# Kernel optimization log

Measured on AMD Instinct MI355X. Metric: run time of the kernel, lower is better.

Reference implementation:

```python
import math
import jax, jax.numpy as jnp
import numpy as np

B, S, D = 8, 1024, 768
N_HEAD, D_HEAD = 12, 64


def setup_inputs() -> dict:
    key = jax.random.key(0)
    k1, k2, k3, k4, k5 = jax.random.split(key, 5)
    return {
        "x": jax.random.normal(k1, (B, S, D), dtype=jnp.float32),
        "W_qkv": jax.random.normal(k2, (D, 3 * D), dtype=jnp.float32) * 0.02,
        "b_qkv": jax.random.normal(k3, (3 * D,), dtype=jnp.float32) * 0.02,
        "W_proj": jax.random.normal(k4, (D, D), dtype=jnp.float32) * 0.02,
        "b_proj": jax.random.normal(k5, (D,), dtype=jnp.float32) * 0.02,
    }


def reference(x, W_qkv, b_qkv, W_proj, b_proj):
    b, s, d = x.shape
    qkv = x @ W_qkv + b_qkv                      # [B,S,3D]
    q, k, v = jnp.split(qkv, 3, axis=-1)
    # [B,S,D] -> [B,H,S,Dh]
    q = q.reshape(b, s, N_HEAD, D_HEAD).transpose(0, 2, 1, 3)
    k = k.reshape(b, s, N_HEAD, D_HEAD).transpose(0, 2, 1, 3)
    v = v.reshape(b, s, N_HEAD, D_HEAD).transpose(0, 2, 1, 3)
    scores = jnp.einsum("bhqd,bhkd->bhqk", q, k) / math.sqrt(D_HEAD)
    causal = jnp.tril(jnp.ones((s, s), dtype=bool))  # [S,S]
    scores = jnp.where(causal[None, None], scores, -jnp.inf)
    probs = jax.nn.softmax(scores, axis=-1)
    out = jnp.einsum("bhqk,bhkd->bhqd", probs, v)    # [B,H,S,Dh]
    out = out.transpose(0, 2, 1, 3).reshape(b, s, d)
    out = out @ W_proj + b_proj
    return out, (k, v)
```

## Files before the change

kernel.cpp:

```cpp
#include <hip/hip_runtime.h>

typedef unsigned short u16;
typedef unsigned int   u32;
typedef short bf16x8 __attribute__((ext_vector_type(8)));
typedef float f32x4  __attribute__((ext_vector_type(4)));
typedef float f32x16 __attribute__((ext_vector_type(16)));
typedef u16   u16x4  __attribute__((ext_vector_type(4)));
typedef u16   u16x8  __attribute__((ext_vector_type(8)));
typedef u32   u32x2  __attribute__((ext_vector_type(2)));
typedef u32   u32x4  __attribute__((ext_vector_type(4)));

#define DEV __device__ __forceinline__
#define MFMA32(A,B,C) __builtin_amdgcn_mfma_f32_32x32x16_bf16(A,B,C,0,0,0)

DEV u16 f2bf(float f) {
  u32 u = __builtin_bit_cast(u32, f);
  u32 r = (u + 0x7FFFu + ((u >> 16) & 1u)) >> 16;
  return (u16)r;
}
DEV u32 pack2(float lo, float hi) {
  return (u32)f2bf(lo) | ((u32)f2bf(hi) << 16);
}
DEV void gll16(const u16* g, u16* l) {
  __builtin_amdgcn_global_load_lds((const __attribute__((address_space(1))) u32*)g,
                                   (__attribute__((address_space(3))) u32*)l,
                                   16, 0, 0);
}

__global__ __launch_bounds__(256)
void cvt_bf16(const float* __restrict__ in, u16* __restrict__ out, int n8) {
  int i = blockIdx.x * 256 + threadIdx.x;
  if (i >= n8) return;
  float4 a = ((const float4*)in)[2*i];
  float4 b = ((const float4*)in)[2*i+1];
  u16x8 o;
  o[0]=f2bf(a.x); o[1]=f2bf(a.y); o[2]=f2bf(a.z); o[3]=f2bf(a.w);
  o[4]=f2bf(b.x); o[5]=f2bf(b.y); o[6]=f2bf(b.z); o[7]=f2bf(b.w);
  *(u16x8*)(out + (size_t)i*8) = o;
}

__global__ __launch_bounds__(256)
void transpose_w(const float* __restrict__ in, u16* __restrict__ out, int R, int C) {
  __shared__ float t64[64][65];
  const int r0 = blockIdx.x*64, c0 = blockIdx.y*64;
  const int tr = threadIdx.x >> 4, tc = (threadIdx.x & 15) * 4;
  #pragma unroll
  for (int i = 0; i < 4; ++i) {
    int r = i*16 + tr;
    float4 v = *(const float4*)(in + (size_t)(r0 + r)*C + c0 + tc);
    t64[r][tc+0]=v.x; t64[r][tc+1]=v.y; t64[r][tc+2]=v.z; t64[r][tc+3]=v.w;
  }
  __syncthreads();
  #pragma unroll
  for (int i = 0; i < 4; ++i) {
    int r = i*16 + tr;
    u16x4 ov;
    ov[0]=f2bf(t64[tc+0][r]); ov[1]=f2bf(t64[tc+1][r]);
    ov[2]=f2bf(t64[tc+2][r]); ov[3]=f2bf(t64[tc+3][r]);
    *(u16x4*)(out + (size_t)(c0 + r)*R + r0 + tc) = ov;
  }
}

template<int MODE>
__global__ __launch_bounds__(256)
void gemm_k(const u16* __restrict__ A, const u16* __restrict__ Bt,
            const float* __restrict__ bias,
            float* __restrict__ o0, float* __restrict__ o1,
            u16* __restrict__ qo, u16* __restrict__ ko)
{
  constexpr int K = 768;
  __shared__ u16 As[128*32];
  __shared__ u16 Bs[128*32];
  const int tid = threadIdx.x;
  const int w  = tid >> 6, ln = tid & 63;
  const int wr = w >> 1,  wc = w & 1;
  const int g  = ln >> 4, c  = ln & 15;
  const int tm = blockIdx.x * 128, tn = blockIdx.y * 128;

  const f32x4 fzero = {0.f, 0.f, 0.f, 0.f};
  f32x4 acc[4][4];
  #pragma unroll
  for (int i = 0; i < 4; ++i)
    #pragma unroll
    for (int j = 0; j < 4; ++j) acc[i][j] = fzero;

  const int srow = w*32 + (ln >> 2);
  const int seg  = (ln & 3) * 8;
  const u16* ga = A  + (size_t)(tm + srow)*K + seg;
  const u16* gb = Bt + (size_t)(tn + srow)*K + seg;
  u16* lA = As + __builtin_amdgcn_readfirstlane(w * 1024);
  u16* lB = Bs + __builtin_amdgcn_readfirstlane(w * 1024);

  for (int k0 = 0; k0 < K; k0 += 32) {
    gll16(ga + k0,        lA);
    gll16(ga + k0 + 16*K, lA + 512);
    gll16(gb + k0,        lB);
    gll16(gb + k0 + 16*K, lB + 512);
    __syncthreads();
    bf16x8 af[4], bfv[4];
    #pragma unroll
    for (int mi = 0; mi < 4; ++mi)
      af[mi] = *(const bf16x8*)&As[(wr*64 + mi*16 + c)*32 + g*8];
    #pragma unroll
    for (int ni = 0; ni < 4; ++ni)
      bfv[ni] = *(const bf16x8*)&Bs[(wc*64 + ni*16 + c)*32 + g*8];
    #pragma unroll
    for (int mi = 0; mi < 4; ++mi)
      #pragma unroll
      for (int ni = 0; ni < 4; ++ni)
        acc[mi][ni] = __builtin_amdgcn_mfma_f32_16x16x32_bf16(af[mi], bfv[ni], acc[mi][ni], 0, 0, 0);
    __syncthreads();
  }

  const int tnw = tn + wc*64;
  float bias_v[4];
  #pragma unroll
  for (int ni = 0; ni < 4; ++ni) bias_v[ni] = bias[tnw + ni*16 + c];

  if (MODE == 1) {
    #pragma unroll
    for (int mi = 0; mi < 4; ++mi)
      #pragma unroll
      for (int r = 0; r < 4; ++r) {
        int mrow = tm + wr*64 + mi*16 + 4*g + r;
        float* op = o0 + (size_t)mrow*768 + tnw + c;
        #pragma unroll
        for (int ni = 0; ni < 4; ++ni)
          op[ni*16] = acc[mi][ni][r] + bias_v[ni];
      }
  } else {
    const float QSCALE = 0.18033688f;
    const int part = tnw / 768;
    const int hh   = (tnw - part*768) >> 6;
    #pragma unroll
    for (int mi = 0; mi < 4; ++mi)
      #pragma unroll
      for (int r = 0; r < 4; ++r) {
        int mrow = tm + wr*64 + mi*16 + 4*g + r;
        int bI = mrow >> 10, s = mrow & 1023;
        size_t base = (((size_t)(bI*12 + hh) << 10) + (size_t)s) * 64 + c;
        #pragma unroll
        for (int ni = 0; ni < 4; ++ni) {
          float v = acc[mi][ni][r] + bias_v[ni];
          size_t idx = base + ni*16;
          if (part == 0)      { qo[idx] = f2bf(v * QSCALE); }
          else if (part == 1) { o0[idx] = v; ko[idx] = f2bf(v); }
          else                { o1[idx] = v; }
        }
      }
  }
}

__global__ __launch_bounds__(256)
void transpose_v(const float* __restrict__ vin, u16* __restrict__ vt) {
  __shared__ float t64[64][65];
  const int bh = blockIdx.x, s0 = blockIdx.y * 64;
  const int tr = threadIdx.x >> 4, tc = (threadIdx.x & 15) * 4;
  const float* src = vin + ((size_t)bh*1024 + s0) * 64;
  #pragma unroll
  for (int i = 0; i < 4; ++i) {
    int r = i*16 + tr;
    float4 v = *(const float4*)(src + (size_t)r*64 + tc);
    t64[r][tc+0]=v.x; t64[r][tc+1]=v.y; t64[r][tc+2]=v.z; t64[r][tc+3]=v.w;
  }
  __syncthreads();
  u16* dst = vt + (size_t)bh*64*1024 + s0;
  #pragma unroll
  for (int i = 0; i < 4; ++i) {
    int d = i*16 + tr;
    u16x4 ov;
    ov[0]=f2bf(t64[tc+0][d]); ov[1]=f2bf(t64[tc+1][d]);
    ov[2]=f2bf(t64[tc+2][d]); ov[3]=f2bf(t64[tc+3][d]);
    *(u16x4*)(dst + (size_t)d*1024 + tc) = ov;
  }
}


#define LOADT(KF, VF, TI) do {                                              \
  const int k32_ = (TI) << 5;                                               \
  const u16* kp_ = kb + hbase + (size_t)(k32_ + cl) * 64 + (hf << 3);       \
  KF[0] = *(const bf16x8*)(kp_);       KF[1] = *(const bf16x8*)(kp_ + 16);  \
  KF[2] = *(const bf16x8*)(kp_ + 32);  KF[3] = *(const bf16x8*)(kp_ + 48);  \
  const u16* vp_ = vt + hbase + (size_t)cl * 1024 + k32_ + (hf << 3);       \
  VF[0] = *(const bf16x8*)(vp_);           VF[1] = *(const bf16x8*)(vp_ + 16); \
  VF[2] = *(const bf16x8*)(vp_ + 32768);   VF[3] = *(const bf16x8*)(vp_ + 32768 + 16); \
} while (0)

#define TILE(KF, VF, DIAG) do {                                             \
  f32x16 st_ = 0.f;                                                         \
  st_ = MFMA32(KF[0], qf[0], st_); st_ = MFMA32(KF[1], qf[1], st_);         \
  st_ = MFMA32(KF[2], qf[2], st_); st_ = MFMA32(KF[3], qf[3], st_);         \
  float x_[16];                                                             \
  _Pragma("unroll")                                                         \
  for (int r = 0; r < 16; ++r) x_[r] = st_[r];                              \
  if (DIAG) {                                                               \
    _Pragma("unroll")                                                       \
    for (int r = 0; r < 16; ++r)                                            \
      if (((r & 3) + 8 * (r >> 2) + (hf << 2)) > cl) x_[r] = -1e30f;        \
  }                                                                         \
  float y_[8];                                                              \
  _Pragma("unroll")                                                         \
  for (int r = 0; r < 8; ++r) y_[r] = fmaxf(x_[r], x_[r + 8]);              \
  _Pragma("unroll")                                                         \
  for (int r = 0; r < 4; ++r) y_[r] = fmaxf(y_[r], y_[r + 4]);              \
  float mt_ = fmaxf(fmaxf(y_[0], y_[1]), fmaxf(y_[2], y_[3]));              \
  mt_ = fmaxf(mt_, __shfl_xor(mt_, 32));                                    \
  if (!__all(mt_ - m <= 8.0f)) {                         \
    float mn_ = fmaxf(m, mt_);                                              \
    float sc_ = exp2f(m - mn_);                                             \
    _Pragma("unroll")                                                       \
    for (int r = 0; r < 16; ++r) { o0[r] *= sc_; o1[r] *= sc_; }            \
    lsum *= sc_; m = mn_;                                                   \
  }                                                                         \
  float p_[16]; float rs_ = 0.f;                                            \
  _Pragma("unroll")                                                         \
  for (int r = 0; r < 16; ++r) { p_[r] = exp2f(x_[r] - m); rs_ += p_[r]; }  \
  rs_ += __shfl_xor(rs_, 32);                                               \
  lsum += rs_;                                                              \
  u32 ww_[8], xw_[8];                                                       \
  _Pragma("unroll")                                                         \
  for (int i = 0; i < 8; ++i) ww_[i] = pack2(p_[2*i], p_[2*i+1]);           \
  _Pragma("unroll")                                                         \
  for (int i = 0; i < 8; ++i) xw_[i] = (u32)__shfl_xor((int)ww_[i], 32);    \
  u32x4 b0_, b1_;                                                           \
  b0_[0] = hf ? xw_[2] : ww_[0]; b0_[1] = hf ? xw_[3] : ww_[1];             \
  b0_[2] = hf ? ww_[2] : xw_[0]; b0_[3] = hf ? ww_[3] : xw_[1];             \
  b1_[0] = hf ? xw_[6] : ww_[4]; b1_[1] = hf ? xw_[7] : ww_[5];             \
  b1_[2] = hf ? ww_[6] : xw_[4]; b1_[3] = hf ? ww_[7] : xw_[5];             \
  bf16x8 pb0_ = __builtin_bit_cast(bf16x8, b0_);                            \
  bf16x8 pb1_ = __builtin_bit_cast(bf16x8, b1_);                            \
  o0 = MFMA32(VF[0], pb0_, o0); o0 = MFMA32(VF[1], pb1_, o0);               \
  o1 = MFMA32(VF[2], pb0_, o1); o1 = MFMA32(VF[3], pb1_, o1);               \
} while (0)

__global__ __launch_bounds__(256)
void attn_k(const u16* __restrict__ qb, const u16* __restrict__ kb,
            const u16* __restrict__ vt, u16* __restrict__ attnb)
{
  const int w = threadIdx.x >> 6, ln = threadIdx.x & 63;
  const int u = blockIdx.x * 4 + w;
  const int head = u % 96;
  const int qt = 31 - (u / 96);
  const int q0 = qt << 5;
  const int b = head / 12, h = head % 12;
  const int cl = ln & 31, hf = ln >> 5;
  const size_t hbase = (size_t)head << 16;

  const u16* Qp = qb + hbase + (size_t)(q0 + cl) * 64 + (hf << 3);
  bf16x8 qf[4];
  qf[0] = *(const bf16x8*)(Qp);       qf[1] = *(const bf16x8*)(Qp + 16);
  qf[2] = *(const bf16x8*)(Qp + 32);  qf[3] = *(const bf16x8*)(Qp + 48);

  f32x16 o0 = 0.f, o1 = 0.f;
  float m = -1e30f, lsum = 0.f;

  bf16x8 kA[4], vA[4], kB[4], vB[4];
  const int nfull = qt;
  LOADT(kA, vA, 0);
  int t = 0;
  while (t < nfull) {
    LOADT(kB, vB, t + 1);
    TILE(kA, vA, 0);
    ++t;
    if (t >= nfull) break;
    LOADT(kA, vA, t + 1);
    TILE(kB, vB, 0);
    ++t;
  }
  if (nfull & 1) TILE(kB, vB, 1);
  else           TILE(kA, vA, 1);

  const float rinv = 1.0f / lsum;
  const size_t obase = ((size_t)(b * 1024 + q0 + cl)) * 768 + h * 64;
  #pragma unroll
  for (int grp = 0; grp < 4; ++grp) {
    u32x2 s0, s1;
    s0[0] = pack2(o0[grp*4+0]*rinv, o0[grp*4+1]*rinv);
    s0[1] = pack2(o0[grp*4+2]*rinv, o0[grp*4+3]*rinv);
    *(u32x2*)(attnb + obase + grp*8 + (hf << 2)) = s0;
    s1[0] = pack2(o1[grp*4+0]*rinv, o1[grp*4+1]*rinv);
    s1[1] = pack2(o1[grp*4+2]*rinv, o1[grp*4+3]*rinv);
    *(u32x2*)(attnb + obase + 32 + grp*8 + (hf << 2)) = s1;
  }
}

extern "C" void kernel_launch(void* const* d_in, const int* in_sizes, int n_in,
                              void* d_out, int out_size, void* d_ws, size_t ws_size,
                              hipStream_t stream)
{
  (void)in_sizes; (void)n_in; (void)out_size; (void)ws_size;
  const float* x     = (const float*)d_in[0];
  const float* Wqkv  = (const float*)d_in[1];
  const float* bqkv  = (const float*)d_in[2];
  const float* Wproj = (const float*)d_in[3];
  const float* bproj = (const float*)d_in[4];
  float* out  = (float*)d_out;
  float* outK = out + 6291456;
  float* outV = out + 2*6291456;

  char* ws = (char*)d_ws;
  u16* xb    = (u16*)ws; ws += 12582912;
  u16* wqt   = (u16*)ws; ws += 3538944;
  u16* wpt   = (u16*)ws; ws += 1179648;
  u16* qbuf  = (u16*)ws; ws += 12582912;
  u16* kbuf  = (u16*)ws; ws += 12582912;
  u16* vtb   = (u16*)ws; ws += 12582912;
  u16* attnb = (u16*)ws; ws += 12582912;

  cvt_bf16   <<<3072, 256, 0, stream>>>(x, xb, 786432);
  transpose_w<<<dim3(12, 36), 256, 0, stream>>>(Wqkv,  wqt, 768, 2304);
  transpose_w<<<dim3(12, 12), 256, 0, stream>>>(Wproj, wpt, 768, 768);
  gemm_k<0>  <<<dim3(64, 18), 256, 0, stream>>>(xb, wqt, bqkv, outK, outV, qbuf, kbuf);
  transpose_v<<<dim3(96, 16), 256, 0, stream>>>(outV, vtb);
  attn_k     <<<768, 256, 0, stream>>>(qbuf, kbuf, vtb, attnb);
  gemm_k<1>  <<<dim3(64, 6),  256, 0, stream>>>(attnb, wpt, bproj, out, nullptr, nullptr, nullptr);
}
```

Measured before the change: 149.0 us.

## Triple-buffer GEMM LDS tiles with async global-to-LDS prefetch two stages ahead

The GEMM main loop now keeps three LDS buffers and issues global_load_lds for tile t+2 while computing tile t. Explicit vmcnt waits and raw s_barrier replace the load-then-sync pattern, so memory latency can overlap the MFMA work. LDS use triples to 48KB per block, which may lower occupancy. Correctness now depends on the hand-written vmcnt counts matching the number of outstanding loads.

```diff
diff --git a/kernel.cpp b/kernel.cpp
--- a/kernel.cpp
+++ b/kernel.cpp
@@ -69,8 +69,9 @@
             u16* __restrict__ qo, u16* __restrict__ ko)
 {
   constexpr int K = 768;
-  __shared__ u16 As[128*32];
-  __shared__ u16 Bs[128*32];
+  constexpr int NT = 24;
+  __shared__ u16 As[3 * 128 * 32];
+  __shared__ u16 Bs[3 * 128 * 32];
   const int tid = threadIdx.x;
   const int w  = tid >> 6, ln = tid & 63;
   const int wr = w >> 1,  wc = w & 1;
@@ -88,29 +89,52 @@
   const int seg  = (ln & 3) * 8;
   const u16* ga = A  + (size_t)(tm + srow)*K + seg;
   const u16* gb = Bt + (size_t)(tn + srow)*K + seg;
-  u16* lA = As + __builtin_amdgcn_readfirstlane(w * 1024);
-  u16* lB = Bs + __builtin_amdgcn_readfirstlane(w * 1024);
-
-  for (int k0 = 0; k0 < K; k0 += 32) {
-    gll16(ga + k0,        lA);
-    gll16(ga + k0 + 16*K, lA + 512);
-    gll16(gb + k0,        lB);
-    gll16(gb + k0 + 16*K, lB + 512);
-    __syncthreads();
+  const int woff = __builtin_amdgcn_readfirstlane(w * 1024);
+
+#define STAGE(P, K0) do {                              \
+    u16* la_ = As + (P)*4096 + woff;                   \
+    u16* lb_ = Bs + (P)*4096 + woff;                   \
+    gll16(ga + (K0),          la_);                    \
+    gll16(ga + (K0) + 16*K,   la_ + 512);              \
+    gll16(gb + (K0),          lb_);                    \
+    gll16(gb + (K0) + 16*K,   lb_ + 512);              \
+  } while (0)
+
+  STAGE(0, 0);
+  STAGE(1, 32);
+  int p = 0;
+  for (int t = 0; t < NT; ++t) {
+    if (t + 2 < NT) {
+      int pn = p + 2; if (pn >= 3) pn -= 3;
+      STAGE(pn, (t + 2) * 32);
+      asm volatile("s_waitcnt vmcnt(8)" ::: "memory");
+    } else if (t + 1 < NT) {
+      asm volatile("s_waitcnt vmcnt(4)" ::: "memory");
+    } else {
+      asm volatile("s_waitcnt vmcnt(0)" ::: "memory");
+    }
+    __builtin_amdgcn_s_barrier();
+
+    const u16* Ab = As + p*4096;
+    const u16* Bb = Bs + p*4096;
     bf16x8 af[4], bfv[4];
     #pragma unroll
     for (int mi = 0; mi < 4; ++mi)
-      af[mi] = *(const bf16x8*)&As[(wr*64 + mi*16 + c)*32 + g*8];
+      af[mi] = *(const bf16x8*)&Ab[(wr*64 + mi*16 + c)*32 + g*8];
     #pragma unroll
     for (int ni = 0; ni < 4; ++ni)
-      bfv[ni] = *(const bf16x8*)&Bs[(wc*64 + ni*16 + c)*32 + g*8];
+      bfv[ni] = *(const bf16x8*)&Bb[(wc*64 + ni*16 + c)*32 + g*8];
     #pragma unroll
     for (int mi = 0; mi < 4; ++mi)
       #pragma unroll
       for (int ni = 0; ni < 4; ++ni)
         acc[mi][ni] = __builtin_amdgcn_mfma_f32_16x16x32_bf16(af[mi], bfv[ni], acc[mi][ni], 0, 0, 0);
-    __syncthreads();
-  }
+
+    asm volatile("" ::: "memory");
+    __builtin_amdgcn_s_barrier();
+    ++p; if (p == 3) p = 0;
+  }
+#undef STAGE
 
   const int tnw = tn + wc*64;
   float bias_v[4];
@@ -175,7 +199,6 @@
   }
 }
 
-
 #define LOADT(KF, VF, TI) do {                                              \
   const int k32_ = (TI) << 5;                                               \
   const u16* kp_ = kb + hbase + (size_t)(k32_ + cl) * 64 + (hf << 3);       \
```

Measured after the change: 154.4 us. 1.04x slower.

## Load GEMM operands directly from global into registers, dropping LDS staging

Applied to the files above, without the earlier changes.

The QKV and projection GEMM no longer stages A and B tiles through shared memory with global_load_lds and two barriers per k-step. Each wave now reads its MFMA fragments straight from global memory in a fully unrolled 24-step loop, and launch bounds request 4 blocks per SM. This removes the barriers and the LDS round trip and lets loads be scheduled ahead of use. In exchange, operand reuse across waves now depends on the L1/L2 caches, and global reads per block rise roughly twofold.

```diff
diff --git a/kernel.cpp b/kernel.cpp
--- a/kernel.cpp
+++ b/kernel.cpp
@@ -20,11 +20,6 @@
 }
 DEV u32 pack2(float lo, float hi) {
   return (u32)f2bf(lo) | ((u32)f2bf(hi) << 16);
-}
-DEV void gll16(const u16* g, u16* l) {
-  __builtin_amdgcn_global_load_lds((const __attribute__((address_space(1))) u32*)g,
-                                   (__attribute__((address_space(3))) u32*)l,
-                                   16, 0, 0);
 }
 
 __global__ __launch_bounds__(256)
@@ -62,15 +57,13 @@
 }
 
 template<int MODE>
-__global__ __launch_bounds__(256)
+__global__ __launch_bounds__(256, 4)
 void gemm_k(const u16* __restrict__ A, const u16* __restrict__ Bt,
             const float* __restrict__ bias,
             float* __restrict__ o0, float* __restrict__ o1,
             u16* __restrict__ qo, u16* __restrict__ ko)
 {
   constexpr int K = 768;
-  __shared__ u16 As[128*32];
-  __shared__ u16 Bs[128*32];
   const int tid = threadIdx.x;
   const int w  = tid >> 6, ln = tid & 63;
   const int wr = w >> 1,  wc = w & 1;
@@ -84,32 +77,27 @@
     #pragma unroll
     for (int j = 0; j < 4; ++j) acc[i][j] = fzero;
 
-  const int srow = w*32 + (ln >> 2);
-  const int seg  = (ln & 3) * 8;
-  const u16* ga = A  + (size_t)(tm + srow)*K + seg;
-  const u16* gb = Bt + (size_t)(tn + srow)*K + seg;
-  u16* lA = As + __builtin_amdgcn_readfirstlane(w * 1024);
-  u16* lB = Bs + __builtin_amdgcn_readfirstlane(w * 1024);
-
-  for (int k0 = 0; k0 < K; k0 += 32) {
-    gll16(ga + k0,        lA);
-    gll16(ga + k0 + 16*K, lA + 512);
-    gll16(gb + k0,        lB);
-    gll16(gb + k0 + 16*K, lB + 512);
-    __syncthreads();
+  const u16* pa[4];
+  const u16* pb[4];
+  #pragma unroll
+  for (int mi = 0; mi < 4; ++mi)
+    pa[mi] = A + (size_t)(tm + wr*64 + mi*16 + c) * K + g*8;
+  #pragma unroll
+  for (int ni = 0; ni < 4; ++ni)
+    pb[ni] = Bt + (size_t)(tn + wc*64 + ni*16 + c) * K + g*8;
+
+  #pragma unroll
+  for (int t = 0; t < 24; ++t) {
     bf16x8 af[4], bfv[4];
     #pragma unroll
-    for (int mi = 0; mi < 4; ++mi)
-      af[mi] = *(const bf16x8*)&As[(wr*64 + mi*16 + c)*32 + g*8];
-    #pragma unroll
-    for (int ni = 0; ni < 4; ++ni)
-      bfv[ni] = *(const bf16x8*)&Bs[(wc*64 + ni*16 + c)*32 + g*8];
+    for (int mi = 0; mi < 4; ++mi) af[mi] = *(const bf16x8*)(pa[mi] + t*32);
+    #pragma unroll
+    for (int ni = 0; ni < 4; ++ni) bfv[ni] = *(const bf16x8*)(pb[ni] + t*32);
     #pragma unroll
     for (int mi = 0; mi < 4; ++mi)
       #pragma unroll
       for (int ni = 0; ni < 4; ++ni)
         acc[mi][ni] = __builtin_amdgcn_mfma_f32_16x16x32_bf16(af[mi], bfv[ni], acc[mi][ni], 0, 0, 0);
-    __syncthreads();
   }
 
   const int tnw = tn + wc*64;
@@ -175,7 +163,6 @@
   }
 }
 
-
 #define LOADT(KF, VF, TI) do {                                              \
   const int k32_ = (TI) << 5;                                               \
   const u16* kp_ = kb + hbase + (size_t)(k32_ + cl) * 64 + (hf << 3);       \
```

Measured after the change: 259.1 us. 1.74x slower.

## Enlarge GEMM tiles to 256x256 with double-buffered LDS staging

Applied to the files above, without the earlier changes.

Both projection GEMMs move from 128x128 tiles with 256 threads to 256x256 tiles with 512 threads. Each K step is now 64 wide, and the next step's global-to-LDS load is issued while the current buffer feeds the MFMAs. The goal is more operand reuse per LDS load and fewer barriers per unit of work, so that load latency is hidden behind compute. In exchange, each block needs 128KB of LDS, so only one block fits per CU. The grids shrink to 288 and 96 blocks, which can leave many CUs idle or create a tail wave, especially for the output projection.

```diff
diff --git a/kernel.cpp b/kernel.cpp
--- a/kernel.cpp
+++ b/kernel.cpp
@@ -62,55 +62,69 @@
 }
 
 template<int MODE>
-__global__ __launch_bounds__(256)
+__global__ __launch_bounds__(512, 2)
 void gemm_k(const u16* __restrict__ A, const u16* __restrict__ Bt,
             const float* __restrict__ bias,
             float* __restrict__ o0, float* __restrict__ o1,
             u16* __restrict__ qo, u16* __restrict__ ko)
 {
   constexpr int K = 768;
-  __shared__ u16 As[128*32];
-  __shared__ u16 Bs[128*32];
+  constexpr int NT = 12;
+  __shared__ u16 As[2 * 16384];
+  __shared__ u16 Bs[2 * 16384];
   const int tid = threadIdx.x;
   const int w  = tid >> 6, ln = tid & 63;
-  const int wr = w >> 1,  wc = w & 1;
+  const int wr = w >> 2,  wc = w & 3;
   const int g  = ln >> 4, c  = ln & 15;
-  const int tm = blockIdx.x * 128, tn = blockIdx.y * 128;
+  const int tm = blockIdx.x * 256, tn = blockIdx.y * 256;
 
   const f32x4 fzero = {0.f, 0.f, 0.f, 0.f};
-  f32x4 acc[4][4];
-  #pragma unroll
-  for (int i = 0; i < 4; ++i)
+  f32x4 acc[8][4];
+  #pragma unroll
+  for (int i = 0; i < 8; ++i)
     #pragma unroll
     for (int j = 0; j < 4; ++j) acc[i][j] = fzero;
 
-  const int srow = w*32 + (ln >> 2);
-  const int seg  = (ln & 3) * 8;
+  const int srow = w*8 + (ln >> 3);
+  const int seg  = (ln & 7) * 8;
   const u16* ga = A  + (size_t)(tm + srow)*K + seg;
   const u16* gb = Bt + (size_t)(tn + srow)*K + seg;
-  u16* lA = As + __builtin_amdgcn_readfirstlane(w * 1024);
-  u16* lB = Bs + __builtin_amdgcn_readfirstlane(w * 1024);
-
-  for (int k0 = 0; k0 < K; k0 += 32) {
-    gll16(ga + k0,        lA);
-    gll16(ga + k0 + 16*K, lA + 512);
-    gll16(gb + k0,        lB);
-    gll16(gb + k0 + 16*K, lB + 512);
+  const int woff = __builtin_amdgcn_readfirstlane(w * 512);
+
+#define STAGE(P, K0) do {                                                 \
+    _Pragma("unroll")                                                     \
+    for (int l = 0; l < 4; ++l) {                                         \
+      gll16(ga + (size_t)l*64*K + (K0), As + (P)*16384 + l*4096 + woff);  \
+      gll16(gb + (size_t)l*64*K + (K0), Bs + (P)*16384 + l*4096 + woff);  \
+    }                                                                     \
+  } while (0)
+
+  STAGE(0, 0);
+  __syncthreads();
+  int cur = 0;
+  for (int t = 0; t < NT; ++t) {
+    if (t + 1 < NT) STAGE(cur ^ 1, (t + 1) * 64);
+    const u16* Ab = As + cur*16384;
+    const u16* Bb = Bs + cur*16384;
+    #pragma unroll
+    for (int ks = 0; ks < 2; ++ks) {
+      bf16x8 af[8], bfv[4];
+      #pragma unroll
+      for (int mi = 0; mi < 8; ++mi)
+        af[mi] = *(const bf16x8*)&Ab[(wr*128 + mi*16 + c)*64 + ks*32 + g*8];
+      #pragma unroll
+      for (int ni = 0; ni < 4; ++ni)
+        bfv[ni] = *(const bf16x8*)&Bb[(wc*64 + ni*16 + c)*64 + ks*32 + g*8];
+      #pragma unroll
+      for (int mi = 0; mi < 8; ++mi)
+        #pragma unroll
+        for (int ni = 0; ni < 4; ++ni)
+          acc[mi][ni] = __builtin_amdgcn_mfma_f32_16x16x32_bf16(af[mi], bfv[ni], acc[mi][ni], 0, 0, 0);
+    }
     __syncthreads();
-    bf16x8 af[4], bfv[4];
-    #pragma unroll
-    for (int mi = 0; mi < 4; ++mi)
-      af[mi] = *(const bf16x8*)&As[(wr*64 + mi*16 + c)*32 + g*8];
-    #pragma unroll
-    for (int ni = 0; ni < 4; ++ni)
-      bfv[ni] = *(const bf16x8*)&Bs[(wc*64 + ni*16 + c)*32 + g*8];
-    #pragma unroll
-    for (int mi = 0; mi < 4; ++mi)
-      #pragma unroll
-      for (int ni = 0; ni < 4; ++ni)
-        acc[mi][ni] = __builtin_amdgcn_mfma_f32_16x16x32_bf16(af[mi], bfv[ni], acc[mi][ni], 0, 0, 0);
-    __syncthreads();
-  }
+    cur ^= 1;
+  }
+#undef STAGE
 
   const int tnw = tn + wc*64;
   float bias_v[4];
@@ -119,10 +133,10 @@
 
   if (MODE == 1) {
     #pragma unroll
-    for (int mi = 0; mi < 4; ++mi)
+    for (int mi = 0; mi < 8; ++mi)
       #pragma unroll
       for (int r = 0; r < 4; ++r) {
-        int mrow = tm + wr*64 + mi*16 + 4*g + r;
+        int mrow = tm + wr*128 + mi*16 + 4*g + r;
         float* op = o0 + (size_t)mrow*768 + tnw + c;
         #pragma unroll
         for (int ni = 0; ni < 4; ++ni)
@@ -133,10 +147,10 @@
     const int part = tnw / 768;
     const int hh   = (tnw - part*768) >> 6;
     #pragma unroll
-    for (int mi = 0; mi < 4; ++mi)
+    for (int mi = 0; mi < 8; ++mi)
       #pragma unroll
       for (int r = 0; r < 4; ++r) {
-        int mrow = tm + wr*64 + mi*16 + 4*g + r;
+        int mrow = tm + wr*128 + mi*16 + 4*g + r;
         int bI = mrow >> 10, s = mrow & 1023;
         size_t base = (((size_t)(bI*12 + hh) << 10) + (size_t)s) * 64 + c;
         #pragma unroll
@@ -175,7 +189,6 @@
   }
 }
 
-
 #define LOADT(KF, VF, TI) do {                                              \
   const int k32_ = (TI) << 5;                                               \
   const u16* kp_ = kb + hbase + (size_t)(k32_ + cl) * 64 + (hf << 3);       \
@@ -216,7 +229,7 @@
   _Pragma("unroll")                                                         \
   for (int r = 0; r < 16; ++r) { p_[r] = exp2f(x_[r] - m); rs_ += p_[r]; }  \
   rs_ += __shfl_xor(rs_, 32);                                               \
-  lsum += rs_;                                                              \
+  lsum += rs_;                                                               \
   u32 ww_[8], xw_[8];                                                       \
   _Pragma("unroll")                                                         \
   for (int i = 0; i < 8; ++i) ww_[i] = pack2(p_[2*i], p_[2*i+1]);           \
@@ -310,8 +323,8 @@
   cvt_bf16   <<<3072, 256, 0, stream>>>(x, xb, 786432);
   transpose_w<<<dim3(12, 36), 256, 0, stream>>>(Wqkv,  wqt, 768, 2304);
   transpose_w<<<dim3(12, 12), 256, 0, stream>>>(Wproj, wpt, 768, 768);
-  gemm_k<0>  <<<dim3(64, 18), 256, 0, stream>>>(xb, wqt, bqkv, outK, outV, qbuf, kbuf);
+  gemm_k<0>  <<<dim3(32, 9), 512, 0, stream>>>(xb, wqt, bqkv, outK, outV, qbuf, kbuf);
   transpose_v<<<dim3(96, 16), 256, 0, stream>>>(outV, vtb);
   attn_k     <<<768, 256, 0, stream>>>(qbuf, kbuf, vtb, attnb);
-  gemm_k<1>  <<<dim3(64, 6),  256, 0, stream>>>(attnb, wpt, bproj, out, nullptr, nullptr, nullptr);
-}
+  gemm_k<1>  <<<dim3(32, 3), 512, 0, stream>>>(attnb, wpt, bproj, out, nullptr, nullptr, nullptr);
+}
```

Result: slower. 190.4 us (+27.8%).
